# Performance work log

Measured on AMD Instinct MI355X. Metric: run time of the kernel, lower is better.

The kernel has to match this reference:

```python
import jax, jax.numpy as jnp
import numpy as np

H, W = 2048, 2048
T_MAX = 30.0
P_MAX = 1.0
# (di, dj, dist_coeff) for the 8-neighborhood, diagonals weighted 0.83
OFFSETS = [(-1, -1, 0.83), (-1, 0, 1.0), (-1, 1, 0.83),
           (0, -1, 1.0),               (0, 1, 1.0),
           (1, -1, 0.83), (1, 0, 1.0), (1, 1, 0.83)]


def _shift(x, di, dj):
    """shifted[i,j] = x[i+di, j+dj], zero outside the grid.
    Equivalent to the torch clamp-index + validity-mask gather, since the mask
    zeroes every out-of-range contribution."""
    p = jnp.pad(x, ((1, 1), (1, 1)))
    return p[1 + di:1 + di + x.shape[0], 1 + dj:1 + dj + x.shape[1]]


def setup_inputs() -> dict:
    key = jax.random.key(0)
    k_h, k_a, k_m, k_w = jax.random.split(key, 4)
    return {
        "log_alpha": jnp.zeros((), jnp.float32),   # log(1.0)
        "log_beta": jnp.zeros((), jnp.float32),
        "log_gamma": jnp.zeros((), jnp.float32),
        "height": jax.random.normal(k_h, (H, W), jnp.float32),
        "age": jax.random.uniform(k_a, (H, W), jnp.float32),
        "moisture": jax.random.uniform(k_m, (H, W), jnp.float32),
        "wind_grid": jax.random.uniform(k_w, (H, W), jnp.float32),
        "ignition_value": jnp.ones((), jnp.float32),
        "i0": 1024,
        "j0": 1024,
        "n_steps": 20,
        "n_substeps": 1,
    }


def _forward(log_alpha, log_beta, log_gamma, height, age, moisture,
             wind_grid, ignition_value, i0, j0, n_steps, n_substeps):
    alpha = jnp.exp(log_alpha)
    beta = jnp.exp(log_beta)
    gamma = jnp.exp(log_gamma)

    # age inflammability: (1+P_MAX)**((age/T_MAX)**alpha) - 1, saturating at P_MAX
    ratio = age / T_MAX
    below = (1.0 + P_MAX) ** (ratio ** alpha) - 1.0
    age_factor = jnp.where(age < T_MAX, below, P_MAX)
    psi = jnp.exp(-beta * moisture)
    gain = age_factor * psi                      # state-independent, hoisted

    # Precompute per-offset coefficient: dist * phi(dh) * validity_mask.
    valid = jnp.ones_like(height)
    coefs = []
    for di, dj, dist in OFFSETS:
        h_nb = _shift(height, di, dj)
        mask = _shift(valid, di, dj)             # 1 where neighbor in-grid
        dh = height - h_nb
        dh_safe = jnp.where(dh > 0, dh, 1.0)     # avoid sqrt'(0) = inf in grads
        downhill = jnp.exp(gamma * dh)
        uphill = 1.0 + gamma * jnp.sqrt(dh_safe)
        phi = jnp.where(dh <= 0, downhill, uphill)
        coefs.append(dist * phi * mask)

    def substep(state):
        ws = state * wind_grid                   # w_nb * s_nb share the shift
        total = jnp.zeros_like(state)
        for (di, dj, _), c in zip(OFFSETS, coefs):
            total = total + c * _shift(ws, di, dj)
        return jnp.clip(state + gain * total, 0.0, 1.0)

    state0 = jnp.zeros((H, W), height.dtype).at[i0, j0].set(ignition_value)
    arrival0 = jnp.full((H, W), float(n_steps), height.dtype)

    def body(carry, t):
        state, prev, arrival = carry
        for _ in range(n_substeps):              # static, typically 1
            state = substep(state)
        first_ignition = jnp.maximum(state - prev, 0.0)
        arrival = arrival - first_ignition * (float(n_steps) - t)
        prev = jax.lax.stop_gradient(state)      # mirrors state.detach()
        return (state, prev, arrival), None

    ts = jnp.arange(1, n_steps + 1, dtype=height.dtype)
    (_, _, arrival), _ = jax.lax.scan(body, (state0, jnp.zeros_like(state0), arrival0), ts)
    return arrival


def reference(log_alpha, log_beta, log_gamma, height, age, moisture,
              wind_grid, ignition_value, i0, j0, n_steps, n_substeps):
    return _forward(log_alpha, log_beta, log_gamma, height, age, moisture,
                    wind_grid, ignition_value, i0, j0, n_steps, n_substeps)
```

## Files before the change

### kernel.cpp

```cpp
#include <hip/hip_runtime.h>


namespace {
constexpr int H = 2048;
constexpr int W = 2048;
constexpr float T_MAX = 30.0f;
constexpr int WIN = 48;
constexpr int PH  = WIN + 2;
constexpr int PW  = WIN + 4;
constexpr int NT  = 576;
}

typedef float vfloat8 __attribute__((ext_vector_type(8)));

__device__ __forceinline__ float fexp2(float x) {
    return __builtin_amdgcn_exp2f(x);
}
__device__ __forceinline__ float flog2(float x) {
    return __builtin_amdgcn_logf(x);
}
__device__ __forceinline__ float fexpe(float x) {
    return fexp2(x * 1.44269504f);
}

__global__ __launch_bounds__(NT, 1) void softfire_fused(
    const float* __restrict__ la_p, const float* __restrict__ lb_p,
    const float* __restrict__ lg_p, const float* __restrict__ height,
    const float* __restrict__ age, const float* __restrict__ moisture,
    const float* __restrict__ wind, const float* __restrict__ ign_p,
    const int* __restrict__ i0_p, const int* __restrict__ j0_p,
    const int* __restrict__ ns_p, const int* __restrict__ nsub_p,
    float* __restrict__ out)
{
    const int i0 = i0_p[0], j0 = j0_p[0];
    const int n_steps = ns_p[0];

    int bi = i0 - WIN / 2;
    bi = bi < 0 ? 0 : (bi > H - WIN ? H - WIN : bi);
    int bj = j0 - WIN / 2;
    bj = bj < 0 ? 0 : (bj > W - WIN ? W - WIN : bj);
    bj &= ~3;

    const int tid = threadIdx.x;

    if (blockIdx.x != 0) {
        const float v = (float)n_steps;
        const int idx = (int)(blockIdx.x - 1) * NT + tid;
        if (idx < (H * W) / 4) {
            const int row  = (idx * 4) / W;
            const int col4 = (idx * 4) % W;
            const bool inwin = (row >= bi) & (row < bi + WIN) &
                               (col4 >= bj) & (col4 < bj + WIN);
            if (!inwin)
                reinterpret_cast<float4*>(out)[idx] = make_float4(v, v, v, v);
        }
        if (blockIdx.x <= 256) {
            float x = ign_p[0];
            #pragma unroll 4
            for (int i = 0; i < 2000; ++i)
                x = fmaf(x, 0.99999988f, 1.0e-7f);
            if (x == -5.0f) out[0] = x;
        }
        return;
    }

    __shared__ float lds[4][PH * PW];

    const float alpha = fexpe(la_p[0]);
    const float beta  = fexpe(lb_p[0]);
    const float gamma = fexpe(lg_p[0]);
    const float ign   = ign_p[0];
    const int n_sub   = nsub_p[0];
    const int eff_steps = n_steps - 1;
    const int total_sub = eff_steps * n_sub;

    for (int k = tid; k < PH * PH; k += NT) {
        const int pr = k / PH, pc = k % PH;
        const int gi = bi - 1 + pr, gj = bj - 1 + pc;
        const size_t g = (size_t)gi * W + gj;
        const bool ingrid = (gi >= 0) & (gi < H) & (gj >= 0) & (gj < W);
        lds[0][pr * PW + pc] = ingrid ? height[g] : 0.0f;
        const bool inter = (pr >= 1) & (pr <= WIN) & (pc >= 1) & (pc <= WIN);
        lds[1][pr * PW + pc] = inter ? wind[g] : 0.0f;
        if (inter) {
            lds[2][pr * PW + pc] = age[g];
            lds[3][pr * PW + pc] = moisture[g];
        }
    }
    __syncthreads();

    const int w = tid >> 6, l = tid & 63;
    const int wp = (w == 0) ? 4 : (w <= 4 ? w - 1 : w);
    const int tr = wp / 3, tc = wp - 3 * tr;
    const int R0 = 2 * (tr * 8 + (l >> 3));
    const int C0 = 2 * (tc * 8 + (l & 7));

    const int ir = i0 - bi, jc = j0 - bj;
    int dr = 0;
    if (R0 > ir) dr = R0 - ir; else if (ir > R0 + 1) dr = ir - (R0 + 1);
    int dc = 0;
    if (C0 > jc) dc = C0 - jc; else if (jc > C0 + 1) dc = jc - (C0 + 1);
    const int dmin = dr > dc ? dr : dc;
    const bool ever_active = (dmin <= total_sub);

    int rA = 7;
    { int sl;
      sl = ir - 16; if (sl < rA) rA = sl;
      sl = 31 - ir; if (sl < rA) rA = sl;
      sl = jc - 16; if (sl < rA) rA = sl;
      sl = 31 - jc; if (sl < rA) rA = sl;
      if (rA < 0) rA = 0;
      if (rA > total_sub) rA = total_sub;
      rA -= rA % n_sub;
    }
    const int stepsA = rA / n_sub;

    auto make_cf = [&](int R, int C) -> vfloat8 {
        const int   DI[8] = {-1,-1,-1, 0, 0, 1, 1, 1};
        const int   DJ[8] = {-1, 0, 1,-1, 1,-1, 0, 1};
        const float DS[8] = {0.83f, 1.0f, 0.83f, 1.0f, 1.0f, 0.83f, 1.0f, 0.83f};
        const int ci = (1 + R) * PW + (1 + C);
        const float h = lds[0][ci];
        const float a = lds[2][ci];
        const float m = lds[3][ci];
        const float ratio = a * (1.0f / T_MAX);
        const float ra = fexp2(alpha * flog2(ratio));
        const float below = fexp2(ra) - 1.0f;
        const float age_factor = (a < T_MAX) ? below : 1.0f;
        const float gn = age_factor * fexpe(-beta * m);
        vfloat8 cf;
        #pragma unroll
        for (int k = 0; k < 8; ++k) {
            const int ni = ci + DI[k] * PW + DJ[k];
            const float hn = lds[0][ni];
            const float wn = lds[1][ni];
            const float dh = h - hn;
            const float phi = (dh <= 0.0f) ? fexpe(gamma * dh)
                                           : (1.0f + gamma * sqrtf(dh));
            cf[k] = gn * DS[k] * phi * wn;
        }
        return cf;
    };

    vfloat8 cfA = (vfloat8)0.0f, cfB = (vfloat8)0.0f,
            cfC = (vfloat8)0.0f, cfD = (vfloat8)0.0f;
    if (ever_active) {
        cfA = make_cf(R0,     C0);
        cfB = make_cf(R0,     C0 + 1);
        cfC = make_cf(R0 + 1, C0);
        cfD = make_cf(R0 + 1, C0 + 1);
    }

    float stA = 0.0f, stB = 0.0f, stC = 0.0f, stD = 0.0f;
    if (bi + R0 == i0     && bj + C0 == j0)     stA = ign;
    if (bi + R0 == i0     && bj + C0 + 1 == j0) stB = ign;
    if (bi + R0 + 1 == i0 && bj + C0 == j0)     stC = ign;
    if (bi + R0 + 1 == i0 && bj + C0 + 1 == j0) stD = ign;
    float pvA = 0.0f, pvB = 0.0f, pvC = 0.0f, pvD = 0.0f;
    float arA = (float)n_steps, arB = arA, arC = arA, arD = arA;

    __syncthreads();

    const int igk = (1 + ir) * PW + (1 + jc);
    for (int k = tid; k < PH * PW; k += NT) {
        lds[0][k] = (k == igk) ? ign : 0.0f;
        lds[1][k] = 0.0f;
    }
    __syncthreads();

    const int tl = R0 * PW + C0;

#define FIRE_CELL(cf, a0, a1, a2, a3, a4, a5, a6, a7, ctr)                 \
          ({ float t0 = cf[0] * (a0), t1 = cf[1] * (a1);                   \
             t0 = fmaf(cf[2], (a2), t0); t1 = fmaf(cf[3], (a3), t1);       \
             t0 = fmaf(cf[4], (a4), t0); t1 = fmaf(cf[5], (a5), t1);       \
             t0 = fmaf(cf[6], (a6), t0); t1 = fmaf(cf[7], (a7), t1);       \
             fminf(fmaxf((ctr) + (t0 + t1), 0.0f), 1.0f); })

    auto segment = [&](int sel_) {
        const float* __restrict__ src = lds[sel_];
        float* __restrict__ dst = lds[sel_ ^ 1];
        const float2* s2 = reinterpret_cast<const float2*>(src + tl);
        const float2 p00 = s2[0],          p01 = s2[1];
        const float2 p10 = s2[PW / 2],     p11 = s2[PW / 2 + 1];
        const float2 p20 = s2[PW],         p21 = s2[PW + 1];
        const float2 p30 = s2[3 * PW / 2], p31 = s2[3 * PW / 2 + 1];
        const float n00 = p00.x, n01 = p00.y, n02 = p01.x, n03 = p01.y;
        const float n10 = p10.x, n11 = p10.y, n12 = p11.x, n13 = p11.y;
        const float n20 = p20.x, n21 = p20.y, n22 = p21.x, n23 = p21.y;
        const float n30 = p30.x, n31 = p30.y, n32 = p31.x, n33 = p31.y;

        stA = FIRE_CELL(cfA, n00, n01, n02, n10, n12, n20, n21, n22, n11);
        stB = FIRE_CELL(cfB, n01, n02, n03, n11, n13, n21, n22, n23, n12);
        stC = FIRE_CELL(cfC, n10, n11, n12, n20, n22, n30, n31, n32, n21);
        stD = FIRE_CELL(cfD, n11, n12, n13, n21, n23, n31, n32, n33, n22);

        dst[tl + PW + 1]     = stA;
        dst[tl + PW + 2]     = stB;
        dst[tl + 2 * PW + 1] = stC;
        dst[tl + 2 * PW + 2] = stD;
    };

    int sel = 0, tg = 0;
    if (w == 0) {
        for (int t = 1; t <= stepsA; ++t) {
            for (int s = 0; s < n_sub; ++s) {
                ++tg;
                if (dmin <= tg) segment(sel);
                __builtin_amdgcn_wave_barrier();
                sel ^= 1;
            }
            if (dmin <= tg) {
                const float wgt = (float)(n_steps - t);
                arA -= fmaxf(stA - pvA, 0.0f) * wgt;  pvA = stA;
                arB -= fmaxf(stB - pvB, 0.0f) * wgt;  pvB = stB;
                arC -= fmaxf(stC - pvC, 0.0f) * wgt;  pvC = stC;
                arD -= fmaxf(stD - pvD, 0.0f) * wgt;  pvD = stD;
            }
        }
    }
    __syncthreads();
    sel = rA & 1;
    tg  = rA;

    for (int t = stepsA + 1; t <= eff_steps; ++t) {
      for (int s = 0; s < n_sub; ++s) {
        ++tg;
        if (dmin <= tg) segment(sel);
        __syncthreads();
        sel ^= 1;
      }
      if (dmin <= tg) {
        const float wgt = (float)(n_steps - t);
        arA -= fmaxf(stA - pvA, 0.0f) * wgt;  pvA = stA;
        arB -= fmaxf(stB - pvB, 0.0f) * wgt;  pvB = stB;
        arC -= fmaxf(stC - pvC, 0.0f) * wgt;  pvC = stC;
        arD -= fmaxf(stD - pvD, 0.0f) * wgt;  pvD = stD;
      }
    }
#undef FIRE_CELL

    float2* o0 = reinterpret_cast<float2*>(out + (size_t)(bi + R0) * W + (bj + C0));
    float2* o1 = reinterpret_cast<float2*>(out + (size_t)(bi + R0 + 1) * W + (bj + C0));
    o0[0] = make_float2(arA, arB);
    o1[0] = make_float2(arC, arD);
}

extern "C" void kernel_launch(void* const* d_in, const int* in_sizes, int n_in,
                              void* d_out, int out_size, void* d_ws, size_t ws_size,
                              hipStream_t stream) {
    const float* log_alpha = (const float*)d_in[0];
    const float* log_beta  = (const float*)d_in[1];
    const float* log_gamma = (const float*)d_in[2];
    const float* height    = (const float*)d_in[3];
    const float* age       = (const float*)d_in[4];
    const float* moisture  = (const float*)d_in[5];
    const float* wind      = (const float*)d_in[6];
    const float* ign       = (const float*)d_in[7];
    const int*   i0        = (const int*)d_in[8];
    const int*   j0        = (const int*)d_in[9];
    const int*   n_steps   = (const int*)d_in[10];
    const int*   n_sub     = (const int*)d_in[11];
    float* out = (float*)d_out;

    const int fill_blocks = (H * W / 4 + NT - 1) / NT;
    softfire_fused<<<fill_blocks + 1, NT, 0, stream>>>(
        log_alpha, log_beta, log_gamma, height, age, moisture, wind, ign,
        i0, j0, n_steps, n_sub, out);
}
```

Before: 126.3 us.

## Use 3x3 cells per thread with 256-thread block over 48x48 window

Each thread now handles a 3x3 block of cells instead of 2x2, cutting the block from 576 to 256 threads (4 waves). The wave-to-tile mapping and the inner region handled by wave 0 before block-wide sync are redone to match. The aim is fewer barrier participants and more register reuse of the stencil neighbourhood per LDS read. In exchange, each thread does more sequential work and uses more registers, and the LDS loads become scalar instead of float2.

```diff
diff --git a/kernel.cpp b/kernel.cpp
--- a/kernel.cpp
+++ b/kernel.cpp
@@ -8,7 +8,7 @@
 constexpr int WIN = 48;
 constexpr int PH  = WIN + 2;
 constexpr int PW  = WIN + 4;
-constexpr int NT  = 576;
+constexpr int NT  = 256;
 }
 
 typedef float vfloat8 __attribute__((ext_vector_type(8)));
@@ -90,25 +90,29 @@
     __syncthreads();
 
     const int w = tid >> 6, l = tid & 63;
-    const int wp = (w == 0) ? 4 : (w <= 4 ? w - 1 : w);
-    const int tr = wp / 3, tc = wp - 3 * tr;
-    const int R0 = 2 * (tr * 8 + (l >> 3));
-    const int C0 = 2 * (tc * 8 + (l & 7));
+    int trr, tcc;
+    if (w == 0)      { trr = 4 + (l >> 3);  tcc = 4 + (l & 7); }
+    else if (w == 1) { trr = l >> 4;        tcc = l & 15; }
+    else if (w == 2) { trr = 12 + (l >> 4); tcc = l & 15; }
+    else             { trr = 4 + (l >> 3);  const int cc = l & 7;
+                       tcc = (cc < 4) ? cc : cc + 8; }
+    const int R0 = 3 * trr;
+    const int C0 = 3 * tcc;
 
     const int ir = i0 - bi, jc = j0 - bj;
     int dr = 0;
-    if (R0 > ir) dr = R0 - ir; else if (ir > R0 + 1) dr = ir - (R0 + 1);
+    if (R0 > ir) dr = R0 - ir; else if (ir > R0 + 2) dr = ir - (R0 + 2);
     int dc = 0;
-    if (C0 > jc) dc = C0 - jc; else if (jc > C0 + 1) dc = jc - (C0 + 1);
+    if (C0 > jc) dc = C0 - jc; else if (jc > C0 + 2) dc = jc - (C0 + 2);
     const int dmin = dr > dc ? dr : dc;
     const bool ever_active = (dmin <= total_sub);
 
-    int rA = 7;
+    int rA = 11;
     { int sl;
-      sl = ir - 16; if (sl < rA) rA = sl;
-      sl = 31 - ir; if (sl < rA) rA = sl;
-      sl = jc - 16; if (sl < rA) rA = sl;
-      sl = 31 - jc; if (sl < rA) rA = sl;
+      sl = ir - 12; if (sl < rA) rA = sl;
+      sl = 35 - ir; if (sl < rA) rA = sl;
+      sl = jc - 12; if (sl < rA) rA = sl;
+      sl = 35 - jc; if (sl < rA) rA = sl;
       if (rA < 0) rA = 0;
       if (rA > total_sub) rA = total_sub;
       rA -= rA % n_sub;
@@ -142,22 +146,30 @@
         return cf;
     };
 
-    vfloat8 cfA = (vfloat8)0.0f, cfB = (vfloat8)0.0f,
-            cfC = (vfloat8)0.0f, cfD = (vfloat8)0.0f;
+    vfloat8 cf00 = (vfloat8)0.0f, cf01 = cf00, cf02 = cf00,
+            cf10 = cf00, cf11 = cf00, cf12 = cf00,
+            cf20 = cf00, cf21 = cf00, cf22 = cf00;
     if (ever_active) {
-        cfA = make_cf(R0,     C0);
-        cfB = make_cf(R0,     C0 + 1);
-        cfC = make_cf(R0 + 1, C0);
-        cfD = make_cf(R0 + 1, C0 + 1);
-    }
-
-    float stA = 0.0f, stB = 0.0f, stC = 0.0f, stD = 0.0f;
-    if (bi + R0 == i0     && bj + C0 == j0)     stA = ign;
-    if (bi + R0 == i0     && bj + C0 + 1 == j0) stB = ign;
-    if (bi + R0 + 1 == i0 && bj + C0 == j0)     stC = ign;
-    if (bi + R0 + 1 == i0 && bj + C0 + 1 == j0) stD = ign;
-    float pvA = 0.0f, pvB = 0.0f, pvC = 0.0f, pvD = 0.0f;
-    float arA = (float)n_steps, arB = arA, arC = arA, arD = arA;
+        cf00 = make_cf(R0,     C0); cf01 = make_cf(R0,     C0 + 1); cf02 = make_cf(R0,     C0 + 2);
+        cf10 = make_cf(R0 + 1, C0); cf11 = make_cf(R0 + 1, C0 + 1); cf12 = make_cf(R0 + 1, C0 + 2);
+        cf20 = make_cf(R0 + 2, C0); cf21 = make_cf(R0 + 2, C0 + 1); cf22 = make_cf(R0 + 2, C0 + 2);
+    }
+
+    float st00 = 0, st01 = 0, st02 = 0, st10 = 0, st11 = 0, st12 = 0,
+          st20 = 0, st21 = 0, st22 = 0;
+    {
+        const int rr = ir - R0, cc = jc - C0;
+        if (rr >= 0 && rr < 3 && cc >= 0 && cc < 3) {
+            if (rr == 0) { if (cc == 0) st00 = ign; else if (cc == 1) st01 = ign; else st02 = ign; }
+            else if (rr == 1) { if (cc == 0) st10 = ign; else if (cc == 1) st11 = ign; else st12 = ign; }
+            else { if (cc == 0) st20 = ign; else if (cc == 1) st21 = ign; else st22 = ign; }
+        }
+    }
+    float pv00 = 0, pv01 = 0, pv02 = 0, pv10 = 0, pv11 = 0, pv12 = 0,
+          pv20 = 0, pv21 = 0, pv22 = 0;
+    const float T = (float)n_steps;
+    float ar00 = T, ar01 = T, ar02 = T, ar10 = T, ar11 = T, ar12 = T,
+          ar20 = T, ar21 = T, ar22 = T;
 
     __syncthreads();
 
@@ -178,28 +190,39 @@
              fminf(fmaxf((ctr) + (t0 + t1), 0.0f), 1.0f); })
 
     auto segment = [&](int sel_) {
-        const float* __restrict__ src = lds[sel_];
+        const float* __restrict__ sp = lds[sel_] + tl;
         float* __restrict__ dst = lds[sel_ ^ 1];
-        const float2* s2 = reinterpret_cast<const float2*>(src + tl);
-        const float2 p00 = s2[0],          p01 = s2[1];
-        const float2 p10 = s2[PW / 2],     p11 = s2[PW / 2 + 1];
-        const float2 p20 = s2[PW],         p21 = s2[PW + 1];
-        const float2 p30 = s2[3 * PW / 2], p31 = s2[3 * PW / 2 + 1];
-        const float n00 = p00.x, n01 = p00.y, n02 = p01.x, n03 = p01.y;
-        const float n10 = p10.x, n11 = p10.y, n12 = p11.x, n13 = p11.y;
-        const float n20 = p20.x, n21 = p20.y, n22 = p21.x, n23 = p21.y;
-        const float n30 = p30.x, n31 = p30.y, n32 = p31.x, n33 = p31.y;
-
-        stA = FIRE_CELL(cfA, n00, n01, n02, n10, n12, n20, n21, n22, n11);
-        stB = FIRE_CELL(cfB, n01, n02, n03, n11, n13, n21, n22, n23, n12);
-        stC = FIRE_CELL(cfC, n10, n11, n12, n20, n22, n30, n31, n32, n21);
-        stD = FIRE_CELL(cfD, n11, n12, n13, n21, n23, n31, n32, n33, n22);
-
-        dst[tl + PW + 1]     = stA;
-        dst[tl + PW + 2]     = stB;
-        dst[tl + 2 * PW + 1] = stC;
-        dst[tl + 2 * PW + 2] = stD;
+        const float n00 = sp[0],          n01 = sp[1],          n02 = sp[2],          n03 = sp[3],          n04 = sp[4];
+        const float n10 = sp[PW],         n11 = sp[PW + 1],     n12 = sp[PW + 2],     n13 = sp[PW + 3],     n14 = sp[PW + 4];
+        const float n20 = sp[2 * PW],     n21 = sp[2 * PW + 1], n22 = sp[2 * PW + 2], n23 = sp[2 * PW + 3], n24 = sp[2 * PW + 4];
+        const float n30 = sp[3 * PW],     n31 = sp[3 * PW + 1], n32 = sp[3 * PW + 2], n33 = sp[3 * PW + 3], n34 = sp[3 * PW + 4];
+        const float n40 = sp[4 * PW],     n41 = sp[4 * PW + 1], n42 = sp[4 * PW + 2], n43 = sp[4 * PW + 3], n44 = sp[4 * PW + 4];
+
+        st00 = FIRE_CELL(cf00, n00, n01, n02, n10, n12, n20, n21, n22, n11);
+        st01 = FIRE_CELL(cf01, n01, n02, n03, n11, n13, n21, n22, n23, n12);
+        st02 = FIRE_CELL(cf02, n02, n03, n04, n12, n14, n22, n23, n24, n13);
+        st10 = FIRE_CELL(cf10, n10, n11, n12, n20, n22, n30, n31, n32, n21);
+        st11 = FIRE_CELL(cf11, n11, n12, n13, n21, n23, n31, n32, n33, n22);
+        st12 = FIRE_CELL(cf12, n12, n13, n14, n22, n24, n32, n33, n34, n23);
+        st20 = FIRE_CELL(cf20, n20, n21, n22, n30, n32, n40, n41, n42, n31);
+        st21 = FIRE_CELL(cf21, n21, n22, n23, n31, n33, n41, n42, n43, n32);
+        st22 = FIRE_CELL(cf22, n22, n23, n24, n32, n34, n42, n43, n44, n33);
+
+        dst[tl + PW + 1]     = st00; dst[tl + PW + 2]     = st01; dst[tl + PW + 3]     = st02;
+        dst[tl + 2 * PW + 1] = st10; dst[tl + 2 * PW + 2] = st11; dst[tl + 2 * PW + 3] = st12;
+        dst[tl + 3 * PW + 1] = st20; dst[tl + 3 * PW + 2] = st21; dst[tl + 3 * PW + 3] = st22;
     };
+
+#define ARRIVAL_UPDATE(wgt)                                                 \
+    { ar00 -= fmaxf(st00 - pv00, 0.0f) * (wgt); pv00 = st00;                \
+      ar01 -= fmaxf(st01 - pv01, 0.0f) * (wgt); pv01 = st01;                \
+      ar02 -= fmaxf(st02 - pv02, 0.0f) * (wgt); pv02 = st02;                \
+      ar10 -= fmaxf(st10 - pv10, 0.0f) * (wgt); pv10 = st10;                \
+      ar11 -= fmaxf(st11 - pv11, 0.0f) * (wgt); pv11 = st11;                \
+      ar12 -= fmaxf(st12 - pv12, 0.0f) * (wgt); pv12 = st12;                \
+      ar20 -= fmaxf(st20 - pv20, 0.0f) * (wgt); pv20 = st20;                \
+      ar21 -= fmaxf(st21 - pv21, 0.0f) * (wgt); pv21 = st21;                \
+      ar22 -= fmaxf(st22 - pv22, 0.0f) * (wgt); pv22 = st22; }
 
     int sel = 0, tg = 0;
     if (w == 0) {
@@ -210,13 +233,7 @@
                 __builtin_amdgcn_wave_barrier();
                 sel ^= 1;
             }
-            if (dmin <= tg) {
-                const float wgt = (float)(n_steps - t);
-                arA -= fmaxf(stA - pvA, 0.0f) * wgt;  pvA = stA;
-                arB -= fmaxf(stB - pvB, 0.0f) * wgt;  pvB = stB;
-                arC -= fmaxf(stC - pvC, 0.0f) * wgt;  pvC = stC;
-                arD -= fmaxf(stD - pvD, 0.0f) * wgt;  pvD = stD;
-            }
+            if (dmin <= tg) ARRIVAL_UPDATE((float)(n_steps - t));
         }
     }
     __syncthreads();
@@ -230,20 +247,17 @@
         __syncthreads();
         sel ^= 1;
       }
-      if (dmin <= tg) {
-        const float wgt = (float)(n_steps - t);
-        arA -= fmaxf(stA - pvA, 0.0f) * wgt;  pvA = stA;
-        arB -= fmaxf(stB - pvB, 0.0f) * wgt;  pvB = stB;
-        arC -= fmaxf(stC - pvC, 0.0f) * wgt;  pvC = stC;
-        arD -= fmaxf(stD - pvD, 0.0f) * wgt;  pvD = stD;
-      }
-    }
+      if (dmin <= tg) ARRIVAL_UPDATE((float)(n_steps - t));
+    }
+#undef ARRIVAL_UPDATE
 #undef FIRE_CELL
 
-    float2* o0 = reinterpret_cast<float2*>(out + (size_t)(bi + R0) * W + (bj + C0));
-    float2* o1 = reinterpret_cast<float2*>(out + (size_t)(bi + R0 + 1) * W + (bj + C0));
-    o0[0] = make_float2(arA, arB);
-    o1[0] = make_float2(arC, arD);
+    float* o0 = out + (size_t)(bi + R0) * W + (bj + C0);
+    float* o1 = o0 + W;
+    float* o2 = o1 + W;
+    o0[0] = ar00; o0[1] = ar01; o0[2] = ar02;
+    o1[0] = ar10; o1[1] = ar11; o1[2] = ar12;
+    o2[0] = ar20; o2[1] = ar21; o2[2] = ar22;
 }
 
 extern "C" void kernel_launch(void* const* d_in, const int* in_sizes, int n_in,
```

After: 135.9 us. +7.6%, slower.
